# Kernel optimization log

Measured on AMD Instinct MI355X. Metric: run time of the kernel, lower is better.

Reference implementation:

```python
import jax, jax.numpy as jnp
import numpy as np

B, S, D = 8, 2048, 128

def setup_inputs() -> dict:
    key = jax.random.key(0)
    kq, kk, kv, km = jax.random.split(key, 4)
    q = jax.random.normal(kq, (B, S, D), dtype=jnp.float32)
    k = jax.random.normal(kk, (B, S, D), dtype=jnp.float32)
    v = jax.random.normal(kv, (B, S, D), dtype=jnp.float32)
    mask = jax.random.randint(km, (B, S), 0, 2).astype(bool)  # True = masked out
    return {"q": q, "k": k, "v": v, "mask": mask}

def reference(q, k, v, mask):
    scaler = np.sqrt(D).astype(np.float32)
    # score[b, i, j] = <q_i, k_j> / sqrt(d_k)
    score = jnp.einsum('bik,bjk->bij', q, k) / scaler
    score = score - jnp.max(score, axis=-1, keepdims=True)
    e = jnp.exp(score)
    # mask is (B, S_kv): broadcast across query positions, zero out masked keys
    e = jnp.where(mask[:, None, :], 0.0, e)
    a = e / jnp.sum(e, axis=-1, keepdims=True)
    c = jnp.einsum('bij,bjd->bid', a, v)
    return c
```

## Files before the change

### kernel.cpp

```cpp
#include <hip/hip_runtime.h>
#include <hip/hip_fp16.h>
#include <math.h>

typedef __attribute__((ext_vector_type(8))) short short8;
typedef __attribute__((ext_vector_type(16))) float floatx16;
typedef __attribute__((ext_vector_type(2))) __bf16 bf16x2;
typedef __attribute__((ext_vector_type(2))) unsigned int uint2v;

namespace {
constexpr int Bn = 8;
constexpr int Sn = 2048;
constexpr int Dn = 128;
constexpr int BQ = 128;
constexpr int BK = 64;
constexpr int QTILES = Sn / BQ;
constexpr int NKB = Sn / BK;
constexpr int ROWS = Bn * Sn;
constexpr int NSPLIT = 4;
constexpr float SC2 = 0.12753102063642597f;
constexpr float DEFER_THR = 8.0f;
constexpr int TILE_USH = BK * Dn;
}

#if __has_builtin(__builtin_amdgcn_exp2f)
#define EXP2(x) __builtin_amdgcn_exp2f(x)
#else
#define EXP2(x) exp2f(x)
#endif

__device__ __forceinline__ unsigned short f2bf(float x) {
  union { float f; unsigned u; } a; a.f = x;
  unsigned r = a.u + 0x7fffu + ((a.u >> 16) & 1u);
  return (unsigned short)(r >> 16);
}

__device__ __forceinline__ unsigned pack2bf(float x, float y) {
  union { bf16x2 b; unsigned u; } c;
  c.b[0] = (__bf16)x; c.b[1] = (__bf16)y;
  return c.u;
}

__device__ __forceinline__ uint2v pl32swap(unsigned a, unsigned b, int h) {
#if __has_builtin(__builtin_amdgcn_permlane32_swap)
  (void)h;
  return __builtin_amdgcn_permlane32_swap(a, b, false, false);
#else
  unsigned ax = __shfl_xor((int)a, 32);
  unsigned bx = __shfl_xor((int)b, 32);
  uint2v r;
  r[0] = h ? bx : a;
  r[1] = h ? b : ax;
  return r;
#endif
}

__device__ __forceinline__ void gl_lds16(const void* g, void* l, int lane) {
#if __has_builtin(__builtin_amdgcn_global_load_lds)
  (void)lane;
  __builtin_amdgcn_global_load_lds((const __attribute__((address_space(1))) unsigned int*)g,
                                   (__attribute__((address_space(3))) unsigned int*)l, 16, 0, 0);
#else
  *(float4*)((char*)l + lane * 16) = *(const float4*)g;
#endif
}

__global__ __launch_bounds__(256)
void prep(const float* __restrict__ kg, const float* __restrict__ vg,
          const unsigned char* __restrict__ mraw,
          unsigned short* __restrict__ Kpg, unsigned short* __restrict__ Vpg,
          float* __restrict__ mb2g) {
  __shared__ __align__(16) float Vf[16 * 136];
  const int p = blockIdx.x;
  const int b = p >> 7, q = p & 127;
  const int kb = q >> 2, k16 = q & 3;
  const int t = threadIdx.x;

  unsigned wv = ((const unsigned int*)mraw)[t];
  int any1  = __syncthreads_or((wv & 0x0000ff00u) ? 1 : 0);
  int any23 = __syncthreads_or((wv & 0xffff0000u) ? 1 : 0);
  const int mlayout = any1 ? 1 : (any23 ? 2 : 0);
  if (p < 64) {
    int idx = p * 256 + t;
    bool ms;
    if (mlayout == 1)      ms = mraw[idx] != 0;
    else if (mlayout == 2) ms = ((const float*)mraw)[idx] != 0.0f;
    else                   ms = ((const int*)mraw)[idx] != 0;
    mb2g[idx] = ms ? -1e30f : 0.0f;
  }

  const int j  = t >> 4;
  const int o8 = t & 15;
  const size_t base = ((size_t)(b * Sn + kb * 64 + k16 * 16 + j)) * 32 + o8 * 2;
  const float4* k4 = (const float4*)kg;
  const float4* v4 = (const float4*)vg;

  {
    float4 a = k4[base], bq = k4[base + 1];
    union { unsigned u[4]; short8 s8; } pk;
    pk.u[0] = pack2bf(a.x, a.y);   pk.u[1] = pack2bf(a.z, a.w);
    pk.u[2] = pack2bf(bq.x, bq.y); pk.u[3] = pack2bf(bq.z, bq.w);
    const int jl = k16 * 16 + j;
    *(short8*)(Kpg + (size_t)(b * NKB + kb) * TILE_USH + jl * 128 + ((o8 ^ (jl & 7)) * 8)) = pk.s8;
  }
  {
    float4 a = v4[base], bq = v4[base + 1];
    *(float4*)&Vf[j * 136 + o8 * 8]     = a;
    *(float4*)&Vf[j * 136 + o8 * 8 + 4] = bq;
  }
  __syncthreads();
  {
    const int d = t >> 1, h = t & 1;
    union { unsigned u[4]; short8 s8; } pv;
    #pragma unroll
    for (int i = 0; i < 4; ++i)
      pv.u[i] = pack2bf(Vf[(h * 8 + 2 * i) * 136 + d], Vf[(h * 8 + 2 * i + 1) * 136 + d]);
    const int og = k16 * 2 + h;
    *(short8*)(Vpg + (size_t)(b * NKB + kb) * TILE_USH + d * 64 + ((og ^ (d & 7)) * 8)) = pv.s8;
  }
}

template<int SPLIT, bool DIRECT>
__global__ __launch_bounds__(256, 2)
void attn_fwd(const float* __restrict__ qg,
              const unsigned short* __restrict__ Kpg,
              const unsigned short* __restrict__ Vpg,
              const float* __restrict__ mb2g,
              float* __restrict__ outg, __half* __restrict__ Op,
              float* __restrict__ Mp, float* __restrict__ Lp) {
  __shared__ __align__(16) unsigned short Khi[2][TILE_USH];
  __shared__ __align__(16) unsigned short Vt[2][TILE_USH];

  const int tid = threadIdx.x;
  const int bid = blockIdx.x;
  const int b   = bid & 7;
  const int q0  = ((bid >> 3) & (QTILES - 1)) * BQ;
  const int s   = bid >> 7;
  const int kb0 = s * (NKB / SPLIT);
  const int kbN = kb0 + NKB / SPLIT;
  const int w   = tid >> 6;
  const int L   = tid & 63;
  const int q   = L & 31;
  const int h   = L >> 5;
  const int sw  = q & 7;

  const char* ktile = (const char*)(Kpg + (size_t)b * NKB * TILE_USH);
  const char* vtile = (const char*)(Vpg + (size_t)b * NKB * TILE_USH);
  const int stagebase = w * 4096;

  short8 qh[8], ql[8];
  {
    const float* qrow = qg + (size_t)(b * Sn + q0 + w * 32 + q) * Dn;
    #pragma unroll
    for (int kstep = 0; kstep < 8; ++kstep) {
      float4 f0 = *(const float4*)(qrow + kstep * 16 + h * 8);
      float4 f1 = *(const float4*)(qrow + kstep * 16 + h * 8 + 4);
      float xs[8] = {f0.x, f0.y, f0.z, f0.w, f1.x, f1.y, f1.z, f1.w};
      #pragma unroll
      for (int j = 0; j < 8; ++j) {
        unsigned short hi = f2bf(xs[j]);
        union { unsigned u; float f; } hv; hv.u = ((unsigned)hi) << 16;
        qh[kstep][j] = (short)hi;
        ql[kstep][j] = (short)f2bf(xs[j] - hv.f);
      }
    }
  }

  float m_i = -INFINITY, l_i = 0.0f;
  float mtrue = -INFINITY;
  floatx16 O32[4];
  #pragma unroll
  for (int dg = 0; dg < 4; ++dg)
    #pragma unroll
    for (int r = 0; r < 16; ++r) O32[dg][r] = 0.0f;

  {
    const char* kt = ktile + (size_t)kb0 * (TILE_USH * 2);
    const char* vt = vtile + (size_t)kb0 * (TILE_USH * 2);
    #pragma unroll
    for (int i = 0; i < 4; ++i) {
      const int off = stagebase + i * 1024;
      gl_lds16(kt + off + L * 16, (char*)Khi[0] + off, L);
      gl_lds16(vt + off + L * 16, (char*)Vt[0] + off, L);
    }
  }

  for (int kb = kb0; kb < kbN; ++kb) {
    const int cur = (kb - kb0) & 1;
    __syncthreads();

    if (kb + 1 < kbN) {
      const char* kt = ktile + (size_t)(kb + 1) * (TILE_USH * 2);
      const char* vt = vtile + (size_t)(kb + 1) * (TILE_USH * 2);
      #pragma unroll
      for (int i = 0; i < 4; ++i) {
        const int off = stagebase + i * 1024;
        gl_lds16(kt + off + L * 16, (char*)Khi[cur ^ 1] + off, L);
        gl_lds16(vt + off + L * 16, (char*)Vt[cur ^ 1] + off, L);
      }
    }

    const unsigned short* Kc = Khi[cur];
    const unsigned short* Vc = Vt[cur];

    const float4* mb4 = (const float4*)(mb2g + b * Sn + kb * BK);
    float4 mbv[2][4];
    #pragma unroll
    for (int kg = 0; kg < 2; ++kg)
      #pragma unroll
      for (int ro = 0; ro < 4; ++ro) mbv[kg][ro] = mb4[kg * 8 + ro * 2 + h];

    floatx16 a32[2];
    #pragma unroll
    for (int kg = 0; kg < 2; ++kg)
      #pragma unroll
      for (int r = 0; r < 16; ++r) a32[kg][r] = 0.0f;
    __builtin_amdgcn_s_setprio(1);
    #pragma unroll
    for (int kstep = 0; kstep < 8; ++kstep) {
      const int ko = ((kstep * 2 + h) ^ sw) * 8;
      #pragma unroll
      for (int kg = 0; kg < 2; ++kg) {
        short8 kf = *(const short8*)&Kc[(kg * 32 + q) * 128 + ko];
        a32[kg] = __builtin_amdgcn_mfma_f32_32x32x16_bf16(kf, qh[kstep], a32[kg], 0, 0, 0);
        a32[kg] = __builtin_amdgcn_mfma_f32_32x32x16_bf16(kf, ql[kstep], a32[kg], 0, 0, 0);
      }
    }
    __builtin_amdgcn_s_setprio(0);

    #pragma unroll
    for (int kg = 0; kg < 2; ++kg)
      #pragma unroll
      for (int ro = 0; ro < 4; ++ro) {
        float4 f = mbv[kg][ro];
        a32[kg][4 * ro + 0] = fmaf(a32[kg][4 * ro + 0], SC2, f.x);
        a32[kg][4 * ro + 1] = fmaf(a32[kg][4 * ro + 1], SC2, f.y);
        a32[kg][4 * ro + 2] = fmaf(a32[kg][4 * ro + 2], SC2, f.z);
        a32[kg][4 * ro + 3] = fmaf(a32[kg][4 * ro + 3], SC2, f.w);
      }
    float mxp[4] = {-INFINITY, -INFINITY, -INFINITY, -INFINITY};
    #pragma unroll
    for (int kg = 0; kg < 2; ++kg)
      #pragma unroll
      for (int r = 0; r < 16; ++r) mxp[r & 3] = fmaxf(mxp[r & 3], a32[kg][r]);
    float mx = fmaxf(fmaxf(mxp[0], mxp[1]), fmaxf(mxp[2], mxp[3]));
    mx = fmaxf(mx, __shfl_xor(mx, 32));
    mtrue = fmaxf(mtrue, mx);

    float mnew;
    if (__all(mx <= m_i + DEFER_THR)) {
      mnew = m_i;
    } else {
      mnew = fmaxf(m_i, mx);
      const float alpha = EXP2(m_i - mnew);
      l_i *= alpha;
      #pragma unroll
      for (int dg = 0; dg < 4; ++dg)
        #pragma unroll
        for (int r = 0; r < 16; ++r) O32[dg][r] *= alpha;
    }

    float rsp[4] = {0.f, 0.f, 0.f, 0.f};
    #pragma unroll
    for (int kg = 0; kg < 2; ++kg)
      #pragma unroll
      for (int r = 0; r < 16; ++r) {
        float e = EXP2(a32[kg][r] - mnew);
        a32[kg][r] = e;
        rsp[r & 3] += e;
      }
    float rs = (rsp[0] + rsp[1]) + (rsp[2] + rsp[3]);
    rs += __shfl_xor(rs, 32);
    l_i += rs;
    m_i = mnew;

    unsigned xw[2][4][2];
    #pragma unroll
    for (int kg = 0; kg < 2; ++kg)
      #pragma unroll
      for (int m = 0; m < 4; ++m) {
        xw[kg][m][0] = pack2bf(a32[kg][4 * m + 0], a32[kg][4 * m + 1]);
        xw[kg][m][1] = pack2bf(a32[kg][4 * m + 2], a32[kg][4 * m + 3]);
      }
    unsigned pfw[4][4];
    #pragma unroll
    for (int kg = 0; kg < 2; ++kg)
      #pragma unroll
      for (int j = 0; j < 2; ++j)
        #pragma unroll
        for (int c2 = 0; c2 < 2; ++c2) {
          uint2v r = pl32swap(xw[kg][2 * j][c2], xw[kg][2 * j + 1][c2], h);
          pfw[kg * 2 + j][c2]     = r[0];
          pfw[kg * 2 + j][2 + c2] = r[1];
        }

    __builtin_amdgcn_s_setprio(1);
    #pragma unroll
    for (int k2 = 0; k2 < 4; ++k2) {
      const int ko = ((k2 * 2 + h) ^ sw) * 8;
      union { unsigned u[4]; short8 s8; } pw;
      pw.u[0] = pfw[k2][0]; pw.u[1] = pfw[k2][1];
      pw.u[2] = pfw[k2][2]; pw.u[3] = pfw[k2][3];
      #pragma unroll
      for (int dg = 0; dg < 4; ++dg) {
        short8 vf = *(const short8*)&Vc[(dg * 32 + q) * 64 + ko];
        O32[dg] = __builtin_amdgcn_mfma_f32_32x32x16_bf16(vf, pw.s8, O32[dg], 0, 0, 0);
      }
    }
    __builtin_amdgcn_s_setprio(0);
  }

  const int row = b * Sn + q0 + w * 32 + q;
  if constexpr (DIRECT) {
    const float inv = 1.0f / l_i;
    float* orow = outg + (size_t)row * Dn;
    #pragma unroll
    for (int dg = 0; dg < 4; ++dg)
      #pragma unroll
      for (int ro = 0; ro < 4; ++ro) {
        float4 f = make_float4(O32[dg][4 * ro] * inv,     O32[dg][4 * ro + 1] * inv,
                               O32[dg][4 * ro + 2] * inv, O32[dg][4 * ro + 3] * inv);
        *(float4*)&orow[dg * 32 + 8 * ro + 4 * h] = f;
      }
  } else {
    const float fin = EXP2(m_i - mtrue);
    __half* orow = Op + ((size_t)s * ROWS + row) * Dn;
    #pragma unroll
    for (int dg = 0; dg < 4; ++dg)
      #pragma unroll
      for (int ro = 0; ro < 4; ++ro) {
        union { __half2 h2[2]; uint2 u; } pk;
        pk.h2[0] = __floats2half2_rn(O32[dg][4 * ro] * fin,     O32[dg][4 * ro + 1] * fin);
        pk.h2[1] = __floats2half2_rn(O32[dg][4 * ro + 2] * fin, O32[dg][4 * ro + 3] * fin);
        *(uint2*)&orow[dg * 32 + 8 * ro + 4 * h] = pk.u;
      }
    if (h == 0) {
      Mp[s * ROWS + row] = mtrue;
      Lp[s * ROWS + row] = l_i * fin;
    }
  }
}

__global__ __launch_bounds__(256)
void attn_combine(const __half* __restrict__ Op, const float* __restrict__ Mp,
                  const float* __restrict__ Lp, float4* __restrict__ out4) {
  const int gid = blockIdx.x * 256 + threadIdx.x;
  const int row = gid >> 5;
  const int c4  = gid & 31;
  float ms[NSPLIT];
  float m = -INFINITY;
  #pragma unroll
  for (int s = 0; s < NSPLIT; ++s) { ms[s] = Mp[s * ROWS + row]; m = fmaxf(m, ms[s]); }
  float l = 0.0f;
  float4 acc = make_float4(0.f, 0.f, 0.f, 0.f);
  #pragma unroll
  for (int s = 0; s < NSPLIT; ++s) {
    float wgt = EXP2(ms[s] - m);
    l = fmaf(Lp[s * ROWS + row], wgt, l);
    union { uint2 u; __half2 h2[2]; } pk;
    pk.u = ((const uint2*)Op)[(size_t)(s * ROWS + row) * 32 + c4];
    float2 f0 = __half22float2(pk.h2[0]);
    float2 f1 = __half22float2(pk.h2[1]);
    acc.x = fmaf(f0.x, wgt, acc.x);
    acc.y = fmaf(f0.y, wgt, acc.y);
    acc.z = fmaf(f1.x, wgt, acc.z);
    acc.w = fmaf(f1.y, wgt, acc.w);
  }
  float inv = 1.0f / l;
  out4[(size_t)row * 32 + c4] = make_float4(acc.x * inv, acc.y * inv, acc.z * inv, acc.w * inv);
}

extern "C" void kernel_launch(void* const* d_in, const int* in_sizes, int n_in,
                              void* d_out, int out_size, void* d_ws, size_t ws_size,
                              hipStream_t stream) {
  const float* q = (const float*)d_in[0];
  const float* k = (const float*)d_in[1];
  const float* v = (const float*)d_in[2];
  const unsigned char* m = (const unsigned char*)d_in[3];
  float* out = (float*)d_out;
  (void)in_sizes; (void)n_in; (void)out_size;

  constexpr size_t OPB = (size_t)NSPLIT * ROWS * Dn * sizeof(__half);
  constexpr size_t MLB = (size_t)NSPLIT * ROWS * sizeof(float);
  constexpr size_t KPB = (size_t)Bn * NKB * TILE_USH * 2;
  constexpr size_t MBB = (size_t)ROWS * sizeof(float);

  char* ws = (char*)d_ws;
  if (ws_size >= OPB + 2 * MLB + 2 * KPB + MBB) {
    __half* Op = (__half*)ws;
    float* Mp = (float*)(ws + OPB);
    float* Lp = (float*)(ws + OPB + MLB);
    unsigned short* Kp = (unsigned short*)(ws + OPB + 2 * MLB);
    unsigned short* Vp = (unsigned short*)(ws + OPB + 2 * MLB + KPB);
    float* mb2 = (float*)(ws + OPB + 2 * MLB + 2 * KPB);
    prep<<<dim3(Bn * NKB * 4), dim3(256), 0, stream>>>(k, v, m, Kp, Vp, mb2);
    attn_fwd<NSPLIT, false><<<dim3(Bn * QTILES * NSPLIT), dim3(256), 0, stream>>>(
        q, Kp, Vp, mb2, out, Op, Mp, Lp);
    attn_combine<<<dim3(ROWS * 32 / 256), dim3(256), 0, stream>>>(
        Op, Mp, Lp, (float4*)out);
  } else if (ws_size >= 2 * KPB + MBB) {
    unsigned short* Kp = (unsigned short*)ws;
    unsigned short* Vp = (unsigned short*)(ws + KPB);
    float* mb2 = (float*)(ws + 2 * KPB);
    prep<<<dim3(Bn * NKB * 4), dim3(256), 0, stream>>>(k, v, m, Kp, Vp, mb2);
    attn_fwd<1, true><<<dim3(Bn * QTILES), dim3(256), 0, stream>>>(
        q, Kp, Vp, mb2, out, nullptr, nullptr, nullptr);
  }
}
```

Measured before the change: 115.4 us.

## Software-pipeline QK^T of next tile with softmax and PV of current tile

Restructures the main loop so the QK^T MFMAs for tile kb+1 are issued before the softmax and PV work of tile kb. K is prefetched two tiles ahead and V one tile ahead, and the loop is unrolled in pairs to ping-pong the score registers and LDS buffers. The goal is to overlap the exp/max VALU work with matrix-core work and hide load latency. It needs a second 32-float score accumulator, which raises register pressure at two waves per SIMD, and it drops the priority hint around QK.

```diff
diff --git a/kernel.cpp b/kernel.cpp
--- a/kernel.cpp
+++ b/kernel.cpp
@@ -119,6 +119,146 @@
   }
 }
 
+
+__device__ __forceinline__ void stage_tile(const char* gsrc, char* ldst,
+                                           int stagebase, int L) {
+  #pragma unroll
+  for (int i = 0; i < 4; ++i) {
+    const int off = stagebase + i * 1024;
+    gl_lds16(gsrc + off + L * 16, ldst + off, L);
+  }
+}
+
+__device__ __forceinline__ void qk_tile(const unsigned short* __restrict__ Kc,
+                                        int q, int h, int sw,
+                                        const short8 (&qh)[8], const short8 (&ql)[8],
+                                        floatx16 (&s)[2]) {
+  #pragma unroll
+  for (int kg = 0; kg < 2; ++kg)
+    #pragma unroll
+    for (int r = 0; r < 16; ++r) s[kg][r] = 0.0f;
+  #pragma unroll
+  for (int kstep = 0; kstep < 8; ++kstep) {
+    const int ko = ((kstep * 2 + h) ^ sw) * 8;
+    #pragma unroll
+    for (int kg = 0; kg < 2; ++kg) {
+      short8 kf = *(const short8*)&Kc[(kg * 32 + q) * 128 + ko];
+      s[kg] = __builtin_amdgcn_mfma_f32_32x32x16_bf16(kf, qh[kstep], s[kg], 0, 0, 0);
+      s[kg] = __builtin_amdgcn_mfma_f32_32x32x16_bf16(kf, ql[kstep], s[kg], 0, 0, 0);
+    }
+  }
+}
+
+__device__ __forceinline__ void tile_body(
+    int kbc, int kbN,
+    const unsigned short* __restrict__ Kread, unsigned short* Kdst,
+    const unsigned short* __restrict__ Vread, unsigned short* Vdst,
+    const char* ktile, const char* vtile, int stagebase, int L,
+    const float* __restrict__ mbrow,
+    int q, int h, int sw,
+    const short8 (&qh)[8], const short8 (&ql)[8],
+    floatx16 (&sCur)[2], floatx16 (&sNxt)[2],
+    floatx16 (&O32)[4], float& m_i, float& l_i, float& mtrue) {
+  __syncthreads();
+
+  if (kbc + 2 < kbN)
+    stage_tile(ktile + (size_t)(kbc + 2) * (TILE_USH * 2), (char*)Kdst, stagebase, L);
+  const bool hasNext = (kbc + 1 < kbN);
+  if (hasNext)
+    stage_tile(vtile + (size_t)(kbc + 1) * (TILE_USH * 2), (char*)Vdst, stagebase, L);
+
+  if (hasNext)
+    qk_tile(Kread, q, h, sw, qh, ql, sNxt);
+
+  const float4* mb4 = (const float4*)(mbrow + kbc * BK);
+  float4 mbv[2][4];
+  #pragma unroll
+  for (int kg = 0; kg < 2; ++kg)
+    #pragma unroll
+    for (int ro = 0; ro < 4; ++ro) mbv[kg][ro] = mb4[kg * 8 + ro * 2 + h];
+
+  #pragma unroll
+  for (int kg = 0; kg < 2; ++kg)
+    #pragma unroll
+    for (int ro = 0; ro < 4; ++ro) {
+      float4 f = mbv[kg][ro];
+      sCur[kg][4 * ro + 0] = fmaf(sCur[kg][4 * ro + 0], SC2, f.x);
+      sCur[kg][4 * ro + 1] = fmaf(sCur[kg][4 * ro + 1], SC2, f.y);
+      sCur[kg][4 * ro + 2] = fmaf(sCur[kg][4 * ro + 2], SC2, f.z);
+      sCur[kg][4 * ro + 3] = fmaf(sCur[kg][4 * ro + 3], SC2, f.w);
+    }
+  float mxp[4] = {-INFINITY, -INFINITY, -INFINITY, -INFINITY};
+  #pragma unroll
+  for (int kg = 0; kg < 2; ++kg)
+    #pragma unroll
+    for (int r = 0; r < 16; ++r) mxp[r & 3] = fmaxf(mxp[r & 3], sCur[kg][r]);
+  float mx = fmaxf(fmaxf(mxp[0], mxp[1]), fmaxf(mxp[2], mxp[3]));
+  mx = fmaxf(mx, __shfl_xor(mx, 32));
+  mtrue = fmaxf(mtrue, mx);
+
+  float mnew;
+  if (__all(mx <= m_i + DEFER_THR)) {
+    mnew = m_i;
+  } else {
+    mnew = fmaxf(m_i, mx);
+    const float alpha = EXP2(m_i - mnew);
+    l_i *= alpha;
+    #pragma unroll
+    for (int dg = 0; dg < 4; ++dg)
+      #pragma unroll
+      for (int r = 0; r < 16; ++r) O32[dg][r] *= alpha;
+  }
+
+  float rsp[4] = {0.f, 0.f, 0.f, 0.f};
+  #pragma unroll
+  for (int kg = 0; kg < 2; ++kg)
+    #pragma unroll
+    for (int r = 0; r < 16; ++r) {
+      float e = EXP2(sCur[kg][r] - mnew);
+      sCur[kg][r] = e;
+      rsp[r & 3] += e;
+    }
+  float rs = (rsp[0] + rsp[1]) + (rsp[2] + rsp[3]);
+  rs += __shfl_xor(rs, 32);
+  l_i += rs;
+  m_i = mnew;
+
+  unsigned xw[2][4][2];
+  #pragma unroll
+  for (int kg = 0; kg < 2; ++kg)
+    #pragma unroll
+    for (int m = 0; m < 4; ++m) {
+      xw[kg][m][0] = pack2bf(sCur[kg][4 * m + 0], sCur[kg][4 * m + 1]);
+      xw[kg][m][1] = pack2bf(sCur[kg][4 * m + 2], sCur[kg][4 * m + 3]);
+    }
+  unsigned pfw[4][4];
+  #pragma unroll
+  for (int kg = 0; kg < 2; ++kg)
+    #pragma unroll
+    for (int j = 0; j < 2; ++j)
+      #pragma unroll
+      for (int c2 = 0; c2 < 2; ++c2) {
+        uint2v r = pl32swap(xw[kg][2 * j][c2], xw[kg][2 * j + 1][c2], h);
+        pfw[kg * 2 + j][c2]     = r[0];
+        pfw[kg * 2 + j][2 + c2] = r[1];
+      }
+
+  __builtin_amdgcn_s_setprio(1);
+  #pragma unroll
+  for (int k2 = 0; k2 < 4; ++k2) {
+    const int ko = ((k2 * 2 + h) ^ sw) * 8;
+    union { unsigned u[4]; short8 s8; } pw;
+    pw.u[0] = pfw[k2][0]; pw.u[1] = pfw[k2][1];
+    pw.u[2] = pfw[k2][2]; pw.u[3] = pfw[k2][3];
+    #pragma unroll
+    for (int dg = 0; dg < 4; ++dg) {
+      short8 vf = *(const short8*)&Vread[(dg * 32 + q) * 64 + ko];
+      O32[dg] = __builtin_amdgcn_mfma_f32_32x32x16_bf16(vf, pw.s8, O32[dg], 0, 0, 0);
+    }
+  }
+  __builtin_amdgcn_s_setprio(0);
+}
+
 template<int SPLIT, bool DIRECT>
 __global__ __launch_bounds__(256, 2)
 void attn_fwd(const float* __restrict__ qg,
@@ -145,6 +285,7 @@
 
   const char* ktile = (const char*)(Kpg + (size_t)b * NKB * TILE_USH);
   const char* vtile = (const char*)(Vpg + (size_t)b * NKB * TILE_USH);
+  const float* mbrow = mb2g + b * Sn;
   const int stagebase = w * 4096;
 
   short8 qh[8], ql[8];
@@ -173,140 +314,22 @@
     #pragma unroll
     for (int r = 0; r < 16; ++r) O32[dg][r] = 0.0f;
 
-  {
-    const char* kt = ktile + (size_t)kb0 * (TILE_USH * 2);
-    const char* vt = vtile + (size_t)kb0 * (TILE_USH * 2);
-    #pragma unroll
-    for (int i = 0; i < 4; ++i) {
-      const int off = stagebase + i * 1024;
-      gl_lds16(kt + off + L * 16, (char*)Khi[0] + off, L);
-      gl_lds16(vt + off + L * 16, (char*)Vt[0] + off, L);
-    }
-  }
-
-  for (int kb = kb0; kb < kbN; ++kb) {
-    const int cur = (kb - kb0) & 1;
-    __syncthreads();
-
-    if (kb + 1 < kbN) {
-      const char* kt = ktile + (size_t)(kb + 1) * (TILE_USH * 2);
-      const char* vt = vtile + (size_t)(kb + 1) * (TILE_USH * 2);
-      #pragma unroll
-      for (int i = 0; i < 4; ++i) {
-        const int off = stagebase + i * 1024;
-        gl_lds16(kt + off + L * 16, (char*)Khi[cur ^ 1] + off, L);
-        gl_lds16(vt + off + L * 16, (char*)Vt[cur ^ 1] + off, L);
-      }
-    }
-
-    const unsigned short* Kc = Khi[cur];
-    const unsigned short* Vc = Vt[cur];
-
-    const float4* mb4 = (const float4*)(mb2g + b * Sn + kb * BK);
-    float4 mbv[2][4];
-    #pragma unroll
-    for (int kg = 0; kg < 2; ++kg)
-      #pragma unroll
-      for (int ro = 0; ro < 4; ++ro) mbv[kg][ro] = mb4[kg * 8 + ro * 2 + h];
-
-    floatx16 a32[2];
-    #pragma unroll
-    for (int kg = 0; kg < 2; ++kg)
-      #pragma unroll
-      for (int r = 0; r < 16; ++r) a32[kg][r] = 0.0f;
-    __builtin_amdgcn_s_setprio(1);
-    #pragma unroll
-    for (int kstep = 0; kstep < 8; ++kstep) {
-      const int ko = ((kstep * 2 + h) ^ sw) * 8;
-      #pragma unroll
-      for (int kg = 0; kg < 2; ++kg) {
-        short8 kf = *(const short8*)&Kc[(kg * 32 + q) * 128 + ko];
-        a32[kg] = __builtin_amdgcn_mfma_f32_32x32x16_bf16(kf, qh[kstep], a32[kg], 0, 0, 0);
-        a32[kg] = __builtin_amdgcn_mfma_f32_32x32x16_bf16(kf, ql[kstep], a32[kg], 0, 0, 0);
-      }
-    }
-    __builtin_amdgcn_s_setprio(0);
-
-    #pragma unroll
-    for (int kg = 0; kg < 2; ++kg)
-      #pragma unroll
-      for (int ro = 0; ro < 4; ++ro) {
-        float4 f = mbv[kg][ro];
-        a32[kg][4 * ro + 0] = fmaf(a32[kg][4 * ro + 0], SC2, f.x);
-        a32[kg][4 * ro + 1] = fmaf(a32[kg][4 * ro + 1], SC2, f.y);
-        a32[kg][4 * ro + 2] = fmaf(a32[kg][4 * ro + 2], SC2, f.z);
-        a32[kg][4 * ro + 3] = fmaf(a32[kg][4 * ro + 3], SC2, f.w);
-      }
-    float mxp[4] = {-INFINITY, -INFINITY, -INFINITY, -INFINITY};
-    #pragma unroll
-    for (int kg = 0; kg < 2; ++kg)
-      #pragma unroll
-      for (int r = 0; r < 16; ++r) mxp[r & 3] = fmaxf(mxp[r & 3], a32[kg][r]);
-    float mx = fmaxf(fmaxf(mxp[0], mxp[1]), fmaxf(mxp[2], mxp[3]));
-    mx = fmaxf(mx, __shfl_xor(mx, 32));
-    mtrue = fmaxf(mtrue, mx);
-
-    float mnew;
-    if (__all(mx <= m_i + DEFER_THR)) {
-      mnew = m_i;
-    } else {
-      mnew = fmaxf(m_i, mx);
-      const float alpha = EXP2(m_i - mnew);
-      l_i *= alpha;
-      #pragma unroll
-      for (int dg = 0; dg < 4; ++dg)
-        #pragma unroll
-        for (int r = 0; r < 16; ++r) O32[dg][r] *= alpha;
-    }
-
-    float rsp[4] = {0.f, 0.f, 0.f, 0.f};
-    #pragma unroll
-    for (int kg = 0; kg < 2; ++kg)
-      #pragma unroll
-      for (int r = 0; r < 16; ++r) {
-        float e = EXP2(a32[kg][r] - mnew);
-        a32[kg][r] = e;
-        rsp[r & 3] += e;
-      }
-    float rs = (rsp[0] + rsp[1]) + (rsp[2] + rsp[3]);
-    rs += __shfl_xor(rs, 32);
-    l_i += rs;
-    m_i = mnew;
-
-    unsigned xw[2][4][2];
-    #pragma unroll
-    for (int kg = 0; kg < 2; ++kg)
-      #pragma unroll
-      for (int m = 0; m < 4; ++m) {
-        xw[kg][m][0] = pack2bf(a32[kg][4 * m + 0], a32[kg][4 * m + 1]);
-        xw[kg][m][1] = pack2bf(a32[kg][4 * m + 2], a32[kg][4 * m + 3]);
-      }
-    unsigned pfw[4][4];
-    #pragma unroll
-    for (int kg = 0; kg < 2; ++kg)
-      #pragma unroll
-      for (int j = 0; j < 2; ++j)
-        #pragma unroll
-        for (int c2 = 0; c2 < 2; ++c2) {
-          uint2v r = pl32swap(xw[kg][2 * j][c2], xw[kg][2 * j + 1][c2], h);
-          pfw[kg * 2 + j][c2]     = r[0];
-          pfw[kg * 2 + j][2 + c2] = r[1];
-        }
-
-    __builtin_amdgcn_s_setprio(1);
-    #pragma unroll
-    for (int k2 = 0; k2 < 4; ++k2) {
-      const int ko = ((k2 * 2 + h) ^ sw) * 8;
-      union { unsigned u[4]; short8 s8; } pw;
-      pw.u[0] = pfw[k2][0]; pw.u[1] = pfw[k2][1];
-      pw.u[2] = pfw[k2][2]; pw.u[3] = pfw[k2][3];
-      #pragma unroll
-      for (int dg = 0; dg < 4; ++dg) {
-        short8 vf = *(const short8*)&Vc[(dg * 32 + q) * 64 + ko];
-        O32[dg] = __builtin_amdgcn_mfma_f32_32x32x16_bf16(vf, pw.s8, O32[dg], 0, 0, 0);
-      }
-    }
-    __builtin_amdgcn_s_setprio(0);
+  stage_tile(ktile + (size_t)kb0 * (TILE_USH * 2), (char*)Khi[0], stagebase, L);
+  stage_tile(vtile + (size_t)kb0 * (TILE_USH * 2), (char*)Vt[0], stagebase, L);
+  __syncthreads();
+  stage_tile(ktile + (size_t)(kb0 + 1) * (TILE_USH * 2), (char*)Khi[1], stagebase, L);
+
+  floatx16 sA[2], sB[2];
+  qk_tile(Khi[0], q, h, sw, qh, ql, sA);
+
+  constexpr int NT = NKB / SPLIT;
+  static_assert((NT & 1) == 0, "pair-pipelined loop needs even tile count");
+  for (int p2 = 0; p2 < NT / 2; ++p2) {
+    const int kb = kb0 + 2 * p2;
+    tile_body(kb, kbN, Khi[1], Khi[0], Vt[0], Vt[1], ktile, vtile, stagebase, L,
+              mbrow, q, h, sw, qh, ql, sA, sB, O32, m_i, l_i, mtrue);
+    tile_body(kb + 1, kbN, Khi[0], Khi[1], Vt[1], Vt[0], ktile, vtile, stagebase, L,
+              mbrow, q, h, sw, qh, ql, sB, sA, O32, m_i, l_i, mtrue);
   }
 
   const int row = b * Sn + q0 + w * 32 + q;
```

Measured after the change: 116.0 us. No clear change (+0.5%).
